# Optimization experiments

Hardware: AMD Instinct MI355X
Metric: run time of the kernel (lower is better)

The kernel has to match this reference:

```python
import jax, jax.numpy as jnp
import numpy as np
import math

B, N, D_IN, D, D_OUT, H = 4, 2048, 128, 128, 256, 4  # D = dim_hidden//2


def _lin(key, din, dout):
    k1, k2 = jax.random.split(key)
    s = 1.0 / math.sqrt(din)
    W = jax.random.uniform(k1, (din, dout), jnp.float32, -s, s)
    b = jax.random.uniform(k2, (dout,), jnp.float32, -s, s)
    return W, b


def setup_inputs() -> dict:
    key = jax.random.key(0)
    ks = jax.random.split(key, 20)
    inp = {"X": jax.random.normal(ks[0], (B, N, D_IN), jnp.float32)}
    # mab dims: (dim_Q, dim_K) -> dim_V=D for each of the 3 MABs
    mab_dims = [(D_IN, D_IN), (D, D), (D, D)]
    ki = 1
    for i, (dq, dk) in enumerate(mab_dims):
        inp[f"m{i}_Wq"], inp[f"m{i}_bq"] = _lin(ks[ki], dq, D); ki += 1
        inp[f"m{i}_Wk"], inp[f"m{i}_bk"] = _lin(ks[ki], dk, D); ki += 1
        inp[f"m{i}_Wv"], inp[f"m{i}_bv"] = _lin(ks[ki], dk, D); ki += 1
        inp[f"m{i}_Wo"], inp[f"m{i}_bo"] = _lin(ks[ki], D, D); ki += 1
    a = math.sqrt(6.0 / (D + 1))  # xavier_uniform for S [1,1,D]
    inp["S"] = jax.random.uniform(ks[ki], (1, 1, D), jnp.float32, -a, a); ki += 1
    inp["pW"], inp["pb"] = _lin(ks[ki], D, D_OUT)
    return inp


def _mab(Q, K, Wq, bq, Wk, bk, Wv, bv, Wo, bo):
    # Linear projections
    Qp = Q @ Wq + bq                       # [B, Nq, D]
    Kp = K @ Wk + bk                       # [B, Nk, D]
    Vp = K @ Wv + bv                       # [B, Nk, D]
    b, nq, dV = Qp.shape
    dh = dV // H
    # torch split(dim_split,2)+cat(0) == head-split on last dim
    Qh = Qp.reshape(b, nq, H, dh)
    Kh = Kp.reshape(b, -1, H, dh)
    Vh = Vp.reshape(b, -1, H, dh)
    # sigmoid attention (no softmax normalizer)
    A = jax.nn.sigmoid(jnp.einsum('bnhd,bmhd->bhnm', Qh, Kh) / jnp.sqrt(jnp.float32(dV)))
    O = Qh + jnp.einsum('bhnm,bmhd->bnhd', A, Vh)
    O = O.reshape(b, nq, dV)
    # residual ReLU-FFN (no LayerNorm since ln=False)
    return O + jax.nn.relu(O @ Wo + bo)


def reference(X,
              m0_Wq, m0_bq, m0_Wk, m0_bk, m0_Wv, m0_bv, m0_Wo, m0_bo,
              m1_Wq, m1_bq, m1_Wk, m1_bk, m1_Wv, m1_bv, m1_Wo, m1_bo,
              m2_Wq, m2_bq, m2_Wk, m2_bk, m2_Wv, m2_bv, m2_Wo, m2_bo,
              S, pW, pb):
    # SAB layer 0: self-attention, dim_in -> D
    Xh = _mab(X, X, m0_Wq, m0_bq, m0_Wk, m0_bk, m0_Wv, m0_bv, m0_Wo, m0_bo)
    # SAB layer 1: D -> D
    Xh = _mab(Xh, Xh, m1_Wq, m1_bq, m1_Wk, m1_bk, m1_Wv, m1_bv, m1_Wo, m1_bo)
    # PMA pooling: seed queries attend over the set
    Sb = jnp.broadcast_to(S, (Xh.shape[0], S.shape[1], S.shape[2]))
    P = _mab(Sb, Xh, m2_Wq, m2_bq, m2_Wk, m2_bk, m2_Wv, m2_bv, m2_Wo, m2_bo)
    # final projection D -> dim_hidden
    return P @ pW + pb  # [B, num_seeds, D_OUT]
```

## Files before the change

### kernel.cpp

```cpp
#include <hip/hip_runtime.h>
#include <hip/hip_bf16.h>

typedef __hip_bfloat16 HB;
typedef __attribute__((ext_vector_type(8))) short short8;
typedef __attribute__((ext_vector_type(4))) short short4v;
typedef __attribute__((ext_vector_type(4))) float f32x4;
typedef __attribute__((ext_vector_type(2))) unsigned int uint2v;
typedef __attribute__((ext_vector_type(4))) unsigned int uint4v;

constexpr int Bn = 4, Nn = 2048, Dm = 128, Hh = 4;
constexpr int MN = Bn * Nn;
constexpr size_t SZ = (size_t)MN * Dm;

static __device__ __forceinline__ short f2bs(float x) {
    __hip_bfloat16 h = __float2bfloat16(x);
    return __builtin_bit_cast(short, h);
}
static __device__ __forceinline__ unsigned short f2bh(float x) {
    return (unsigned short)((__builtin_bit_cast(unsigned int, x) + 0x8000u) >> 16);
}
static __device__ __forceinline__ unsigned int pk2(float lo, float hi) {
    unsigned int a = __builtin_bit_cast(unsigned int, lo) + 0x8000u;
    unsigned int b = __builtin_bit_cast(unsigned int, hi) + 0x8000u;
#if __has_builtin(__builtin_amdgcn_perm)
    return __builtin_amdgcn_perm(b, a, 0x07060302u);
#else
    return (a >> 16) | (b & 0xFFFF0000u);
#endif
}
static __device__ __forceinline__ float ex2(float x) {
#if __has_builtin(__builtin_amdgcn_exp2f)
    return __builtin_amdgcn_exp2f(x);
#else
    return exp2f(x);
#endif
}
#define NSC2 (-0.12751884772864078f)

static __device__ __forceinline__ size_t kh_idx(int row, int col) {
    return ((size_t)((row >> 11) * 4 + (col >> 5)) * 2048 + (row & 2047)) * 32 + (col & 31);
}

__global__ void k_wprep(const float* __restrict__ Wa, const float* __restrict__ Wb,
                        const float* __restrict__ Wc, const float* __restrict__ Wd,
                        const float* __restrict__ We, const float* __restrict__ Wf,
                        const float* __restrict__ Wg, const float* __restrict__ Wh,
                        const float* __restrict__ Wi, const float* __restrict__ Wj,
                        HB* __restrict__ WtAll) {
    const float* src;
    switch (blockIdx.x) {
        case 0: src = Wa; break; case 1: src = Wb; break;
        case 2: src = Wc; break; case 3: src = Wd; break;
        case 4: src = We; break; case 5: src = Wf; break;
        case 6: src = Wg; break; case 7: src = Wh; break;
        case 8: src = Wi; break; default: src = Wj; break;
    }
    HB* dst = WtAll + (size_t)blockIdx.x * 16384;
    #pragma unroll
    for (int it = 0; it < 2; ++it) {
        int idx = blockIdx.y * 512 + it * 256 + threadIdx.x;
        int g = idx >> 7, c = idx & 127;
        short8 p;
        #pragma unroll
        for (int j = 0; j < 8; ++j) p[j] = f2bs(src[(size_t)(g * 8 + j) * 128 + c]);
        *(short8*)((short*)dst + (size_t)idx * 8) = p;
    }
}

template<int NW, int RELU, int NEXTRA, int FUSE>
__global__ __launch_bounds__(512) void k_linm(
        const float* __restrict__ A, const float* __restrict__ extra,
        const HB* __restrict__ Wt0, const float* __restrict__ b0,
        const HB* __restrict__ Wt1, const float* __restrict__ b1,
        const HB* __restrict__ Wt2, const float* __restrict__ b2,
        float* __restrict__ C0, float* __restrict__ C1,
        HB* __restrict__ Qb, HB* __restrict__ Kb, HB* __restrict__ Vt) {
    const int tid = threadIdx.x;
    const int w = tid >> 6, lane = tid & 63, l15 = lane & 15, quad = lane >> 4;
    const int row0 = blockIdx.x * 32 + (w >> 2) * 16;
    const int cbase = (w & 3) * 32;

    short8 af[4];
    #pragma unroll
    for (int kc = 0; kc < 4; ++kc) {
        const float* ap = A + (size_t)(row0 + l15) * 128 + kc * 32 + quad * 8;
        float4 x0 = *(const float4*)ap;
        float4 x1 = *(const float4*)(ap + 4);
        if (NEXTRA) {
            const float* ep = extra + (size_t)(row0 + l15) * 128 + kc * 32 + quad * 8;
            float4 e0 = *(const float4*)ep, e1 = *(const float4*)(ep + 4);
            x0.x += e0.x; x0.y += e0.y; x0.z += e0.z; x0.w += e0.w;
            x1.x += e1.x; x1.y += e1.y; x1.z += e1.z; x1.w += e1.w;
        }
        uint4v u;
        u[0] = pk2(x0.x, x0.y); u[1] = pk2(x0.z, x0.w);
        u[2] = pk2(x1.x, x1.y); u[3] = pk2(x1.z, x1.w);
        af[kc] = __builtin_bit_cast(short8, u);
    }

    f32x4 zero = {0.f, 0.f, 0.f, 0.f};
    #pragma unroll
    for (int ct = 0; ct < 2; ++ct) {
        const int col = cbase + ct * 16 + l15;
        #pragma unroll
        for (int s = 0; s < NW; ++s) {
            const HB* Wt = (s == 0) ? Wt0 : (s == 1) ? Wt1 : Wt2;
            const float* bs = (s == 0) ? b0 : (s == 1) ? b1 : b2;
            f32x4 acc = zero;
            #pragma unroll
            for (int kc = 0; kc < 4; ++kc) {
                short8 bf = *(const short8*)((const short*)Wt + ((size_t)(kc * 4 + quad) * 128 + col) * 8);
                acc = __builtin_amdgcn_mfma_f32_16x16x32_bf16(af[kc], bf, acc, 0, 0, 0);
            }
            float bb = bs[col];
            if (s == 0 || !FUSE) {
                float* Cs = (s == 0) ? C0 : C1;
                #pragma unroll
                for (int r = 0; r < 4; ++r) {
                    int row = row0 + quad * 4 + r;
                    float v = acc[r] + bb;
                    if (RELU && s == 0) {
                        float st = A[(size_t)row * 128 + col];
                        if (NEXTRA) st += extra[(size_t)row * 128 + col];
                        v = fmaxf(v, 0.f) + st;
                    }
                    Cs[(size_t)row * 128 + col] = v;
                    if (FUSE && s == 0)
                        ((unsigned short*)Qb)[(size_t)row * 128 + col] = f2bh(v);
                }
            } else if (s == 1) {
                #pragma unroll
                for (int r = 0; r < 4; ++r) {
                    int row = row0 + quad * 4 + r;
                    ((unsigned short*)Kb)[kh_idx(row, col)] = f2bh(acc[r] + bb);
                }
            } else {
                int b_ = row0 >> 11;
                int mloc = (row0 + quad * 4) & 2047;
                int slotb = (mloc & ~31) + (((mloc & 15) >> 2) << 3) + (((mloc >> 4) & 1) << 2);
                int h_ = col >> 5, dh = col & 31;
                uint2v pv;
                pv[0] = pk2(acc[0] + bb, acc[1] + bb);
                pv[1] = pk2(acc[2] + bb, acc[3] + bb);
                *(short4v*)((short*)Vt + ((size_t)((b_ * 4 + h_) * 32 + dh)) * 2048 + slotb)
                    = __builtin_bit_cast(short4v, pv);
            }
        }
    }
}

template<int NQKV, int FUSE>
__global__ __launch_bounds__(512) void k_fused(
        const float* __restrict__ A, const float* __restrict__ extra,
        const HB* __restrict__ WtO, const float* __restrict__ bO,
        const HB* __restrict__ Wt0, const float* __restrict__ b0,
        const HB* __restrict__ Wt1, const float* __restrict__ b1,
        const HB* __restrict__ Wt2, const float* __restrict__ b2,
        float* __restrict__ C0, float* __restrict__ C1,
        HB* __restrict__ Qb, HB* __restrict__ Kb, HB* __restrict__ Vt) {
    const int tid = threadIdx.x;
    const int w = tid >> 6, lane = tid & 63, l15 = lane & 15, quad = lane >> 4;
    const int lrow0 = (w >> 2) * 16;
    const int row0 = blockIdx.x * 32 + lrow0;
    const int cbase = (w & 3) * 32;

    __shared__ float xs[32 * 132];

    short8 af[4];
    #pragma unroll
    for (int kc = 0; kc < 4; ++kc) {
        const float* ap = A + (size_t)(row0 + l15) * 128 + kc * 32 + quad * 8;
        float4 x0 = *(const float4*)ap;
        float4 x1 = *(const float4*)(ap + 4);
        const float* ep = extra + (size_t)(row0 + l15) * 128 + kc * 32 + quad * 8;
        float4 e0 = *(const float4*)ep, e1 = *(const float4*)(ep + 4);
        x0.x += e0.x; x0.y += e0.y; x0.z += e0.z; x0.w += e0.w;
        x1.x += e1.x; x1.y += e1.y; x1.z += e1.z; x1.w += e1.w;
        uint4v u;
        u[0] = pk2(x0.x, x0.y); u[1] = pk2(x0.z, x0.w);
        u[2] = pk2(x1.x, x1.y); u[3] = pk2(x1.z, x1.w);
        af[kc] = __builtin_bit_cast(short8, u);
    }

    f32x4 zero = {0.f, 0.f, 0.f, 0.f};

    #pragma unroll
    for (int ct = 0; ct < 2; ++ct) {
        const int col = cbase + ct * 16 + l15;
        f32x4 acc = zero;
        #pragma unroll
        for (int kc = 0; kc < 4; ++kc) {
            short8 bf = *(const short8*)((const short*)WtO + ((size_t)(kc * 4 + quad) * 128 + col) * 8);
            acc = __builtin_amdgcn_mfma_f32_16x16x32_bf16(af[kc], bf, acc, 0, 0, 0);
        }
        float bb = bO[col];
        #pragma unroll
        for (int r = 0; r < 4; ++r) {
            int row = row0 + quad * 4 + r;
            float st = A[(size_t)row * 128 + col] + extra[(size_t)row * 128 + col];
            xs[(lrow0 + quad * 4 + r) * 132 + col] = fmaxf(acc[r] + bb, 0.f) + st;
        }
    }
    __syncthreads();

    short8 a2[4];
    {
        const float* xrow = xs + (size_t)(lrow0 + l15) * 132;
        #pragma unroll
        for (int kc = 0; kc < 4; ++kc) {
            f32x4 x0 = *(const f32x4*)(xrow + kc * 32 + quad * 8);
            f32x4 x1 = *(const f32x4*)(xrow + kc * 32 + quad * 8 + 4);
            uint4v u;
            u[0] = pk2(x0[0], x0[1]); u[1] = pk2(x0[2], x0[3]);
            u[2] = pk2(x1[0], x1[1]); u[3] = pk2(x1[2], x1[3]);
            a2[kc] = __builtin_bit_cast(short8, u);
        }
    }

    #pragma unroll
    for (int ct = 0; ct < 2; ++ct) {
        const int col = cbase + ct * 16 + l15;
        #pragma unroll
        for (int s = 0; s < NQKV; ++s) {
            const HB* Wt = (s == 0) ? Wt0 : (s == 1) ? Wt1 : Wt2;
            const float* bs = (s == 0) ? b0 : (s == 1) ? b1 : b2;
            f32x4 acc = zero;
            #pragma unroll
            for (int kc = 0; kc < 4; ++kc) {
                short8 bf = *(const short8*)((const short*)Wt + ((size_t)(kc * 4 + quad) * 128 + col) * 8);
                acc = __builtin_amdgcn_mfma_f32_16x16x32_bf16(a2[kc], bf, acc, 0, 0, 0);
            }
            float bb = bs[col];
            if (s == 0 || !FUSE) {
                float* Cs = (s == 0) ? C0 : C1;
                #pragma unroll
                for (int r = 0; r < 4; ++r) {
                    int row = row0 + quad * 4 + r;
                    float v = acc[r] + bb;
                    Cs[(size_t)row * 128 + col] = v;
                    if (FUSE && s == 0)
                        ((unsigned short*)Qb)[(size_t)row * 128 + col] = f2bh(v);
                }
            } else if (s == 1) {
                #pragma unroll
                for (int r = 0; r < 4; ++r) {
                    int row = row0 + quad * 4 + r;
                    ((unsigned short*)Kb)[kh_idx(row, col)] = f2bh(acc[r] + bb);
                }
            } else {
                int b_ = row0 >> 11;
                int mloc = (row0 + quad * 4) & 2047;
                int slotb = (mloc & ~31) + (((mloc & 15) >> 2) << 3) + (((mloc >> 4) & 1) << 2);
                int h_ = col >> 5, dh = col & 31;
                uint2v pv;
                pv[0] = pk2(acc[0] + bb, acc[1] + bb);
                pv[1] = pk2(acc[2] + bb, acc[3] + bb);
                *(short4v*)((short*)Vt + ((size_t)((b_ * 4 + h_) * 32 + dh)) * 2048 + slotb)
                    = __builtin_bit_cast(short4v, pv);
            }
        }
    }
}

__global__ __launch_bounds__(512, 4) void k_attn4(const HB* __restrict__ Qb, const HB* __restrict__ Kbf,
                                                  const HB* __restrict__ Vt, float* __restrict__ Opart) {
    const int tid = threadIdx.x;
    const int w = tid >> 6, lane = tid & 63, l15 = lane & 15, quad = lane >> 4;
    const int bh = blockIdx.x & 15, qg2 = blockIdx.x >> 4;
    const int b = bh >> 2, h = bh & 3;
    const int q0row = qg2 * 64;

    __shared__ float ldsacc[8][64][36];

    short8 aq[4];
    {
        const short* qp = (const short*)Qb + (size_t)(b * Nn + q0row) * 128 + h * 32 + quad * 8;
        #pragma unroll
        for (int qa = 0; qa < 4; ++qa)
            aq[qa] = *(const short8*)(qp + (size_t)(qa * 16 + l15) * 128);
    }

    f32x4 zero = {0.f, 0.f, 0.f, 0.f};
    f32x4 o[4][2];
    #pragma unroll
    for (int qa = 0; qa < 4; ++qa) { o[qa][0] = zero; o[qa][1] = zero; }

    const short* Kb = (const short*)Kbf + (size_t)bh * Nn * 32;
    const short* Vb = (const short*)Vt + (size_t)bh * 32 * Nn;

    for (int m0 = w * 256; m0 < w * 256 + 256; m0 += 64) {
        short8 kb[4];
        #pragma unroll
        for (int mc = 0; mc < 4; ++mc)
            kb[mc] = *(const short8*)(Kb + (size_t)(m0 + mc * 16 + l15) * 32 + quad * 8);
        short8 vf[2][2];
        #pragma unroll
        for (int t = 0; t < 2; ++t)
            #pragma unroll
            for (int u = 0; u < 2; ++u)
                vf[t][u] = *(const short8*)(Vb + (size_t)(t * 16 + l15) * Nn + m0 + u * 32 + quad * 8);

        #pragma unroll
        for (int qa = 0; qa < 4; ++qa) {
            f32x4 s[4];
            #pragma unroll
            for (int mc = 0; mc < 4; ++mc)
                s[mc] = __builtin_amdgcn_mfma_f32_16x16x32_bf16(kb[mc], aq[qa], zero, 0, 0, 0);
            #pragma unroll
            for (int u = 0; u < 2; ++u) {
                f32x4 lo = s[2 * u], hi = s[2 * u + 1];
                float p0 = __builtin_amdgcn_rcpf(1.f + ex2(lo[0] * NSC2));
                float p1 = __builtin_amdgcn_rcpf(1.f + ex2(lo[1] * NSC2));
                float p2 = __builtin_amdgcn_rcpf(1.f + ex2(lo[2] * NSC2));
                float p3 = __builtin_amdgcn_rcpf(1.f + ex2(lo[3] * NSC2));
                float p4 = __builtin_amdgcn_rcpf(1.f + ex2(hi[0] * NSC2));
                float p5 = __builtin_amdgcn_rcpf(1.f + ex2(hi[1] * NSC2));
                float p6 = __builtin_amdgcn_rcpf(1.f + ex2(hi[2] * NSC2));
                float p7 = __builtin_amdgcn_rcpf(1.f + ex2(hi[3] * NSC2));
                uint4v pu;
                pu[0] = pk2(p0, p1); pu[1] = pk2(p2, p3);
                pu[2] = pk2(p4, p5); pu[3] = pk2(p6, p7);
                short8 pf = __builtin_bit_cast(short8, pu);
                #pragma unroll
                for (int t = 0; t < 2; ++t)
                    o[qa][t] = __builtin_amdgcn_mfma_f32_16x16x32_bf16(vf[t][u], pf, o[qa][t], 0, 0, 0);
            }
        }
    }

    #pragma unroll
    for (int qa = 0; qa < 4; ++qa)
        #pragma unroll
        for (int t = 0; t < 2; ++t)
            *(f32x4*)&ldsacc[w][qa * 16 + l15][t * 16 + quad * 4] = o[qa][t];
    __syncthreads();
    const int row = tid >> 3, cc = (tid & 7) * 4;
    f32x4 sum = zero;
    #pragma unroll
    for (int ww = 0; ww < 8; ++ww) {
        f32x4 r = *(f32x4*)&ldsacc[ww][row][cc];
        sum += r;
    }
    *(f32x4*)(Opart + (size_t)(b * Nn + q0row + row) * 128 + h * 32 + cc) = sum;
}

__global__ void k_pma2(const float* __restrict__ S, const float* __restrict__ Wq, const float* __restrict__ bq,
                       const float* __restrict__ Kp, const float* __restrict__ Vp,
                       float* __restrict__ P0part) {
    const int bh = blockIdx.x, b = bh >> 2, h = bh & 3;
    const int ms = blockIdx.y;
    const int tid = threadIdx.x;
    __shared__ float4 qs4[8];
    float* qs = (float*)qs4;
    if (tid < 32) {
        float a = bq[h * 32 + tid];
        for (int k = 0; k < 128; ++k)
            a = fmaf(S[k], Wq[k * Dm + h * 32 + tid], a);
        qs[tid] = a;
    }
    __syncthreads();

    float4 q[8];
    #pragma unroll
    for (int i = 0; i < 8; ++i) q[i] = qs4[i];

    const size_t base = (size_t)b * Nn * Dm + h * 32;
    const int m = ms * 256 + tid;

    const float4* kp = (const float4*)(Kp + base + (size_t)m * Dm);
    const float4* vp = (const float4*)(Vp + base + (size_t)m * Dm);
    float d0 = 0.f, d1 = 0.f, d2 = 0.f, d3 = 0.f;
    #pragma unroll
    for (int c = 0; c < 8; c += 4) {
        float4 k0 = kp[c+0], k1 = kp[c+1], k2 = kp[c+2], k3 = kp[c+3];
        d0 += q[c+0].x*k0.x + q[c+0].y*k0.y + q[c+0].z*k0.z + q[c+0].w*k0.w;
        d1 += q[c+1].x*k1.x + q[c+1].y*k1.y + q[c+1].z*k1.z + q[c+1].w*k1.w;
        d2 += q[c+2].x*k2.x + q[c+2].y*k2.y + q[c+2].z*k2.z + q[c+2].w*k2.w;
        d3 += q[c+3].x*k3.x + q[c+3].y*k3.y + q[c+3].z*k3.z + q[c+3].w*k3.w;
    }
    float dot = (d0 + d1) + (d2 + d3);
    float a = __builtin_amdgcn_rcpf(1.f + ex2(dot * NSC2));
    float4 acc[8];
    #pragma unroll
    for (int c = 0; c < 8; ++c) {
        float4 vv = vp[c];
        acc[c].x = a * vv.x; acc[c].y = a * vv.y; acc[c].z = a * vv.z; acc[c].w = a * vv.w;
    }
    #pragma unroll
    for (int off = 1; off < 64; off <<= 1) {
        #pragma unroll
        for (int c = 0; c < 8; ++c) {
            acc[c].x += __shfl_xor(acc[c].x, off);
            acc[c].y += __shfl_xor(acc[c].y, off);
            acc[c].z += __shfl_xor(acc[c].z, off);
            acc[c].w += __shfl_xor(acc[c].w, off);
        }
    }
    __shared__ float red[4][32];
    const int wave = tid >> 6, lane = tid & 63;
    if (lane == 0) {
        #pragma unroll
        for (int c = 0; c < 8; ++c) {
            red[wave][c*4+0] = acc[c].x; red[wave][c*4+1] = acc[c].y;
            red[wave][c*4+2] = acc[c].z; red[wave][c*4+3] = acc[c].w;
        }
    }
    __syncthreads();
    if (tid < 32) {
        float t = (red[0][tid] + red[1][tid]) + (red[2][tid] + red[3][tid]);
        if (ms == 0) t += qs[tid];
        P0part[ms * 512 + b * 128 + h * 32 + tid] = t;
    }
}

__global__ __launch_bounds__(256) void k_tail(const float* __restrict__ P0part,
                                              const float* __restrict__ W23, const float* __restrict__ b23,
                                              const float* __restrict__ pW, const float* __restrict__ pb,
                                              float* __restrict__ out) {
    const int b = blockIdx.x, tid = threadIdx.x;
    __shared__ float staged[128], pp[128];
    if (tid < 128) {
        float s = 0.f;
        #pragma unroll
        for (int ms = 0; ms < 8; ++ms) s += P0part[ms * 512 + b * 128 + tid];
        staged[tid] = s;
    }
    __syncthreads();
    if (tid < 128) {
        float acc = b23[tid];
        #pragma unroll 8
        for (int k = 0; k < 128; ++k)
            acc = fmaf(staged[k], W23[k * 128 + tid], acc);
        pp[tid] = fmaxf(acc, 0.f) + staged[tid];
    }
    __syncthreads();
    float a = pb[tid];
    #pragma unroll 8
    for (int k = 0; k < 128; ++k)
        a = fmaf(pp[k], pW[k * 256 + tid], a);
    out[b * 256 + tid] = a;
}

extern "C" void kernel_launch(void* const* d_in, const int* in_sizes, int n_in,
                              void* d_out, int out_size, void* d_ws, size_t ws_size,
                              hipStream_t stream) {
    const float* X = (const float*)d_in[0];
    auto W = [&](int i) { return (const float*)d_in[i]; };
    float* ws = (float*)d_ws;

    float* s0 = ws + 0 * SZ;
    float* s1 = ws + 1 * SZ;
    float* s2 = ws + 2 * SZ;
    float* s3 = ws + 3 * SZ;
    HB*    B4  = (HB*)(ws + 4 * SZ);
    HB*    Qb  = B4;
    HB*    Kbf = B4 + SZ;
    HB*    Vt  = B4 + 2 * SZ;
    HB*    WtAll = B4 + 3 * SZ;
    auto Wt = [&](int idx) { return (const HB*)(WtAll + (size_t)idx * 16384); };
    float* P0part = s1;

    const int GLM = MN / 32;
    const int attn_blocks = 512;
    dim3 wprep_grid(10, 4);
    dim3 pma_grid(Bn * Hh, 8);
    const float* nul = nullptr;

    k_wprep<<<wprep_grid, 256, 0, stream>>>(W(1), W(3), W(5), W(7), W(9), W(11), W(13), W(15),
                                            W(19), W(21), WtAll);

    k_linm<3,0,0,1><<<GLM, 512, 0, stream>>>(X, nul, Wt(0), W(2), Wt(1), W(4), Wt(2), W(6),
                                             s0, nullptr, Qb, Kbf, Vt);
    k_attn4<<<attn_blocks, 512, 0, stream>>>(Qb, Kbf, Vt, s2);

    k_fused<3,1><<<GLM, 512, 0, stream>>>(s0, s2, Wt(3), W(8),
                                          Wt(4), W(10), Wt(5), W(12), Wt(6), W(14),
                                          s1, nullptr, Qb, Kbf, Vt);
    k_attn4<<<attn_blocks, 512, 0, stream>>>(Qb, Kbf, Vt, s2);

    k_fused<2,0><<<GLM, 512, 0, stream>>>(s1, s2, Wt(7), W(16),
                                          Wt(8), W(20), Wt(9), W(22), nullptr, nul,
                                          s0, s3, nullptr, nullptr, nullptr);

    k_pma2<<<pma_grid, 256, 0, stream>>>((const float*)d_in[25], W(17), W(18), s0, s3, P0part);
    k_tail<<<Bn, 256, 0, stream>>>(P0part, W(23), W(24), (const float*)d_in[26], (const float*)d_in[27],
                                   (float*)d_out);
}
```

Before: 208.5 us.

## Split fused FFN+QKV kernels into smaller linear kernels with bf16 intermediate

Replaces the fused Wo-FFN plus next-layer projection kernels with two launches of a generic linear kernel. The new kernel uses 16-row blocks with a column-split grid and 256 threads, which raises the block count for more parallelism. The FFN output is stored as bf16 and read directly as the MFMA A operand. This adds two kernel launches and a global round trip for the intermediate in exchange for more blocks and less per-block work. The PMA kernel now uses blockIdx.y directly in place of the ms variable.

```diff
diff --git a/kernel.cpp b/kernel.cpp
--- a/kernel.cpp
+++ b/kernel.cpp
@@ -67,197 +67,106 @@
     }
 }
 
-template<int NW, int RELU, int NEXTRA, int FUSE>
-__global__ __launch_bounds__(512) void k_linm(
-        const float* __restrict__ A, const float* __restrict__ extra,
+template<int NW, int NEXTRA, int FUSE, int ABF, int OUTB>
+__global__ __launch_bounds__(256) void k_lin2(
+        const void* __restrict__ Av, const float* __restrict__ extra,
         const HB* __restrict__ Wt0, const float* __restrict__ b0,
         const HB* __restrict__ Wt1, const float* __restrict__ b1,
         const HB* __restrict__ Wt2, const float* __restrict__ b2,
         float* __restrict__ C0, float* __restrict__ C1,
-        HB* __restrict__ Qb, HB* __restrict__ Kb, HB* __restrict__ Vt) {
+        HB* __restrict__ Xb, HB* __restrict__ Qb, HB* __restrict__ Kb, HB* __restrict__ Vt) {
     const int tid = threadIdx.x;
     const int w = tid >> 6, lane = tid & 63, l15 = lane & 15, quad = lane >> 4;
-    const int row0 = blockIdx.x * 32 + (w >> 2) * 16;
-    const int cbase = (w & 3) * 32;
+    const int row0 = blockIdx.x * 16;
+    const int col = blockIdx.y * 64 + w * 16 + l15;
+    const float* Af = (const float*)Av;
 
     short8 af[4];
-    #pragma unroll
-    for (int kc = 0; kc < 4; ++kc) {
-        const float* ap = A + (size_t)(row0 + l15) * 128 + kc * 32 + quad * 8;
-        float4 x0 = *(const float4*)ap;
-        float4 x1 = *(const float4*)(ap + 4);
-        if (NEXTRA) {
-            const float* ep = extra + (size_t)(row0 + l15) * 128 + kc * 32 + quad * 8;
-            float4 e0 = *(const float4*)ep, e1 = *(const float4*)(ep + 4);
-            x0.x += e0.x; x0.y += e0.y; x0.z += e0.z; x0.w += e0.w;
-            x1.x += e1.x; x1.y += e1.y; x1.z += e1.z; x1.w += e1.w;
-        }
-        uint4v u;
-        u[0] = pk2(x0.x, x0.y); u[1] = pk2(x0.z, x0.w);
-        u[2] = pk2(x1.x, x1.y); u[3] = pk2(x1.z, x1.w);
-        af[kc] = __builtin_bit_cast(short8, u);
+    if (ABF) {
+        const short* ab = (const short*)Av + (size_t)(row0 + l15) * 128 + quad * 8;
+        #pragma unroll
+        for (int kc = 0; kc < 4; ++kc)
+            af[kc] = *(const short8*)(ab + kc * 32);
+    } else {
+        #pragma unroll
+        for (int kc = 0; kc < 4; ++kc) {
+            const float* ap = Af + (size_t)(row0 + l15) * 128 + kc * 32 + quad * 8;
+            float4 x0 = *(const float4*)ap;
+            float4 x1 = *(const float4*)(ap + 4);
+            if (NEXTRA) {
+                const float* ep = extra + (size_t)(row0 + l15) * 128 + kc * 32 + quad * 8;
+                float4 e0 = *(const float4*)ep, e1 = *(const float4*)(ep + 4);
+                x0.x += e0.x; x0.y += e0.y; x0.z += e0.z; x0.w += e0.w;
+                x1.x += e1.x; x1.y += e1.y; x1.z += e1.z; x1.w += e1.w;
+            }
+            uint4v u;
+            u[0] = pk2(x0.x, x0.y); u[1] = pk2(x0.z, x0.w);
+            u[2] = pk2(x1.x, x1.y); u[3] = pk2(x1.z, x1.w);
+            af[kc] = __builtin_bit_cast(short8, u);
+        }
     }
 
     f32x4 zero = {0.f, 0.f, 0.f, 0.f};
     #pragma unroll
-    for (int ct = 0; ct < 2; ++ct) {
-        const int col = cbase + ct * 16 + l15;
-        #pragma unroll
-        for (int s = 0; s < NW; ++s) {
-            const HB* Wt = (s == 0) ? Wt0 : (s == 1) ? Wt1 : Wt2;
-            const float* bs = (s == 0) ? b0 : (s == 1) ? b1 : b2;
-            f32x4 acc = zero;
-            #pragma unroll
-            for (int kc = 0; kc < 4; ++kc) {
-                short8 bf = *(const short8*)((const short*)Wt + ((size_t)(kc * 4 + quad) * 128 + col) * 8);
-                acc = __builtin_amdgcn_mfma_f32_16x16x32_bf16(af[kc], bf, acc, 0, 0, 0);
-            }
-            float bb = bs[col];
-            if (s == 0 || !FUSE) {
-                float* Cs = (s == 0) ? C0 : C1;
+    for (int s = 0; s < NW; ++s) {
+        const HB* Wt = (s == 0) ? Wt0 : (s == 1) ? Wt1 : Wt2;
+        const float* bs = (s == 0) ? b0 : (s == 1) ? b1 : b2;
+        f32x4 acc = zero;
+        #pragma unroll
+        for (int kc = 0; kc < 4; ++kc) {
+            short8 bf = *(const short8*)((const short*)Wt + ((size_t)(kc * 4 + quad) * 128 + col) * 8);
+            acc = __builtin_amdgcn_mfma_f32_16x16x32_bf16(af[kc], bf, acc, 0, 0, 0);
+        }
+        float bb = bs[col];
+        if (s == 0) {
+            if (OUTB) {
+                #pragma unroll
+                for (int r = 0; r < 4; ++r) {
+                    int row = row0 + quad * 4 + r;
+                    float st = Af[(size_t)row * 128 + col];
+                    if (NEXTRA) st += extra[(size_t)row * 128 + col];
+                    float v = fmaxf(acc[r] + bb, 0.f) + st;
+                    ((unsigned short*)Xb)[(size_t)row * 128 + col] = f2bh(v);
+                }
+            } else if (FUSE) {
                 #pragma unroll
                 for (int r = 0; r < 4; ++r) {
                     int row = row0 + quad * 4 + r;
                     float v = acc[r] + bb;
-                    if (RELU && s == 0) {
-                        float st = A[(size_t)row * 128 + col];
-                        if (NEXTRA) st += extra[(size_t)row * 128 + col];
-                        v = fmaxf(v, 0.f) + st;
-                    }
-                    Cs[(size_t)row * 128 + col] = v;
-                    if (FUSE && s == 0)
-                        ((unsigned short*)Qb)[(size_t)row * 128 + col] = f2bh(v);
+                    C0[(size_t)row * 128 + col] = v;
+                    ((unsigned short*)Qb)[(size_t)row * 128 + col] = f2bh(v);
                 }
-            } else if (s == 1) {
+            } else {
+                #pragma unroll
+                for (int r = 0; r < 4; ++r) {
+                    int row = row0 + quad * 4 + r;
+                    C0[(size_t)row * 128 + col] = acc[r] + bb;
+                }
+            }
+        } else if (s == 1) {
+            if (FUSE) {
                 #pragma unroll
                 for (int r = 0; r < 4; ++r) {
                     int row = row0 + quad * 4 + r;
                     ((unsigned short*)Kb)[kh_idx(row, col)] = f2bh(acc[r] + bb);
                 }
             } else {
-                int b_ = row0 >> 11;
-                int mloc = (row0 + quad * 4) & 2047;
-                int slotb = (mloc & ~31) + (((mloc & 15) >> 2) << 3) + (((mloc >> 4) & 1) << 2);
-                int h_ = col >> 5, dh = col & 31;
-                uint2v pv;
-                pv[0] = pk2(acc[0] + bb, acc[1] + bb);
-                pv[1] = pk2(acc[2] + bb, acc[3] + bb);
-                *(short4v*)((short*)Vt + ((size_t)((b_ * 4 + h_) * 32 + dh)) * 2048 + slotb)
-                    = __builtin_bit_cast(short4v, pv);
-            }
-        }
-    }
-}
-
-template<int NQKV, int FUSE>
-__global__ __launch_bounds__(512) void k_fused(
-        const float* __restrict__ A, const float* __restrict__ extra,
-        const HB* __restrict__ WtO, const float* __restrict__ bO,
-        const HB* __restrict__ Wt0, const float* __restrict__ b0,
-        const HB* __restrict__ Wt1, const float* __restrict__ b1,
-        const HB* __restrict__ Wt2, const float* __restrict__ b2,
-        float* __restrict__ C0, float* __restrict__ C1,
-        HB* __restrict__ Qb, HB* __restrict__ Kb, HB* __restrict__ Vt) {
-    const int tid = threadIdx.x;
-    const int w = tid >> 6, lane = tid & 63, l15 = lane & 15, quad = lane >> 4;
-    const int lrow0 = (w >> 2) * 16;
-    const int row0 = blockIdx.x * 32 + lrow0;
-    const int cbase = (w & 3) * 32;
-
-    __shared__ float xs[32 * 132];
-
-    short8 af[4];
-    #pragma unroll
-    for (int kc = 0; kc < 4; ++kc) {
-        const float* ap = A + (size_t)(row0 + l15) * 128 + kc * 32 + quad * 8;
-        float4 x0 = *(const float4*)ap;
-        float4 x1 = *(const float4*)(ap + 4);
-        const float* ep = extra + (size_t)(row0 + l15) * 128 + kc * 32 + quad * 8;
-        float4 e0 = *(const float4*)ep, e1 = *(const float4*)(ep + 4);
-        x0.x += e0.x; x0.y += e0.y; x0.z += e0.z; x0.w += e0.w;
-        x1.x += e1.x; x1.y += e1.y; x1.z += e1.z; x1.w += e1.w;
-        uint4v u;
-        u[0] = pk2(x0.x, x0.y); u[1] = pk2(x0.z, x0.w);
-        u[2] = pk2(x1.x, x1.y); u[3] = pk2(x1.z, x1.w);
-        af[kc] = __builtin_bit_cast(short8, u);
-    }
-
-    f32x4 zero = {0.f, 0.f, 0.f, 0.f};
-
-    #pragma unroll
-    for (int ct = 0; ct < 2; ++ct) {
-        const int col = cbase + ct * 16 + l15;
-        f32x4 acc = zero;
-        #pragma unroll
-        for (int kc = 0; kc < 4; ++kc) {
-            short8 bf = *(const short8*)((const short*)WtO + ((size_t)(kc * 4 + quad) * 128 + col) * 8);
-            acc = __builtin_amdgcn_mfma_f32_16x16x32_bf16(af[kc], bf, acc, 0, 0, 0);
-        }
-        float bb = bO[col];
-        #pragma unroll
-        for (int r = 0; r < 4; ++r) {
-            int row = row0 + quad * 4 + r;
-            float st = A[(size_t)row * 128 + col] + extra[(size_t)row * 128 + col];
-            xs[(lrow0 + quad * 4 + r) * 132 + col] = fmaxf(acc[r] + bb, 0.f) + st;
-        }
-    }
-    __syncthreads();
-
-    short8 a2[4];
-    {
-        const float* xrow = xs + (size_t)(lrow0 + l15) * 132;
-        #pragma unroll
-        for (int kc = 0; kc < 4; ++kc) {
-            f32x4 x0 = *(const f32x4*)(xrow + kc * 32 + quad * 8);
-            f32x4 x1 = *(const f32x4*)(xrow + kc * 32 + quad * 8 + 4);
-            uint4v u;
-            u[0] = pk2(x0[0], x0[1]); u[1] = pk2(x0[2], x0[3]);
-            u[2] = pk2(x1[0], x1[1]); u[3] = pk2(x1[2], x1[3]);
-            a2[kc] = __builtin_bit_cast(short8, u);
-        }
-    }
-
-    #pragma unroll
-    for (int ct = 0; ct < 2; ++ct) {
-        const int col = cbase + ct * 16 + l15;
-        #pragma unroll
-        for (int s = 0; s < NQKV; ++s) {
-            const HB* Wt = (s == 0) ? Wt0 : (s == 1) ? Wt1 : Wt2;
-            const float* bs = (s == 0) ? b0 : (s == 1) ? b1 : b2;
-            f32x4 acc = zero;
-            #pragma unroll
-            for (int kc = 0; kc < 4; ++kc) {
-                short8 bf = *(const short8*)((const short*)Wt + ((size_t)(kc * 4 + quad) * 128 + col) * 8);
-                acc = __builtin_amdgcn_mfma_f32_16x16x32_bf16(a2[kc], bf, acc, 0, 0, 0);
-            }
-            float bb = bs[col];
-            if (s == 0 || !FUSE) {
-                float* Cs = (s == 0) ? C0 : C1;
                 #pragma unroll
                 for (int r = 0; r < 4; ++r) {
                     int row = row0 + quad * 4 + r;
-                    float v = acc[r] + bb;
-                    Cs[(size_t)row * 128 + col] = v;
-                    if (FUSE && s == 0)
-                        ((unsigned short*)Qb)[(size_t)row * 128 + col] = f2bh(v);
+                    C1[(size_t)row * 128 + col] = acc[r] + bb;
                 }
-            } else if (s == 1) {
-                #pragma unroll
-                for (int r = 0; r < 4; ++r) {
-                    int row = row0 + quad * 4 + r;
-                    ((unsigned short*)Kb)[kh_idx(row, col)] = f2bh(acc[r] + bb);
-                }
-            } else {
-                int b_ = row0 >> 11;
-                int mloc = (row0 + quad * 4) & 2047;
-                int slotb = (mloc & ~31) + (((mloc & 15) >> 2) << 3) + (((mloc >> 4) & 1) << 2);
-                int h_ = col >> 5, dh = col & 31;
-                uint2v pv;
-                pv[0] = pk2(acc[0] + bb, acc[1] + bb);
-                pv[1] = pk2(acc[2] + bb, acc[3] + bb);
-                *(short4v*)((short*)Vt + ((size_t)((b_ * 4 + h_) * 32 + dh)) * 2048 + slotb)
-                    = __builtin_bit_cast(short4v, pv);
             }
+        } else {
+            int b_ = row0 >> 11;
+            int mloc = (row0 + quad * 4) & 2047;
+            int slotb = (mloc & ~31) + (((mloc & 15) >> 2) << 3) + (((mloc >> 4) & 1) << 2);
+            int h_ = col >> 5, dh = col & 31;
+            uint2v pv;
+            pv[0] = pk2(acc[0] + bb, acc[1] + bb);
+            pv[1] = pk2(acc[2] + bb, acc[3] + bb);
+            *(short4v*)((short*)Vt + ((size_t)((b_ * 4 + h_) * 32 + dh)) * 2048 + slotb)
+                = __builtin_bit_cast(short4v, pv);
         }
     }
 }
@@ -365,7 +274,7 @@
     for (int i = 0; i < 8; ++i) q[i] = qs4[i];
 
     const size_t base = (size_t)b * Nn * Dm + h * 32;
-    const int m = ms * 256 + tid;
+    const int m = blockIdx.y * 256 + tid;
 
     const float4* kp = (const float4*)(Kp + base + (size_t)m * Dm);
     const float4* vp = (const float4*)(Vp + base + (size_t)m * Dm);
@@ -408,8 +317,8 @@
     __syncthreads();
     if (tid < 32) {
         float t = (red[0][tid] + red[1][tid]) + (red[2][tid] + red[3][tid]);
-        if (ms == 0) t += qs[tid];
-        P0part[ms * 512 + b * 128 + h * 32 + tid] = t;
+        if (blockIdx.y == 0) t += qs[tid];
+        P0part[blockIdx.y * 512 + b * 128 + h * 32 + tid] = t;
     }
 }
 
@@ -456,31 +365,35 @@
     HB*    Qb  = B4;
     HB*    Kbf = B4 + SZ;
     HB*    Vt  = B4 + 2 * SZ;
-    HB*    WtAll = B4 + 3 * SZ;
+    HB*    Xb  = B4 + 3 * SZ;
+    HB*    WtAll = B4 + 4 * SZ;
     auto Wt = [&](int idx) { return (const HB*)(WtAll + (size_t)idx * 16384); };
     float* P0part = s1;
 
-    const int GLM = MN / 32;
+    dim3 lin_grid(MN / 16, 2);
     const int attn_blocks = 512;
     dim3 wprep_grid(10, 4);
     dim3 pma_grid(Bn * Hh, 8);
     const float* nul = nullptr;
+    HB* nulh = nullptr;
 
     k_wprep<<<wprep_grid, 256, 0, stream>>>(W(1), W(3), W(5), W(7), W(9), W(11), W(13), W(15),
                                             W(19), W(21), WtAll);
 
-    k_linm<3,0,0,1><<<GLM, 512, 0, stream>>>(X, nul, Wt(0), W(2), Wt(1), W(4), Wt(2), W(6),
-                                             s0, nullptr, Qb, Kbf, Vt);
+    k_lin2<3,0,1,0,0><<<lin_grid, 256, 0, stream>>>(X, nul, Wt(0), W(2), Wt(1), W(4), Wt(2), W(6),
+                                                    s0, nullptr, nulh, Qb, Kbf, Vt);
     k_attn4<<<attn_blocks, 512, 0, stream>>>(Qb, Kbf, Vt, s2);
-
-    k_fused<3,1><<<GLM, 512, 0, stream>>>(s0, s2, Wt(3), W(8),
-                                          Wt(4), W(10), Wt(5), W(12), Wt(6), W(14),
-                                          s1, nullptr, Qb, Kbf, Vt);
+    k_lin2<1,1,0,0,1><<<lin_grid, 256, 0, stream>>>(s0, s2, Wt(3), W(8), nullptr, nul, nullptr, nul,
+                                                    nullptr, nullptr, Xb, nulh, nulh, nulh);
+
+    k_lin2<3,0,1,1,0><<<lin_grid, 256, 0, stream>>>(Xb, nul, Wt(4), W(10), Wt(5), W(12), Wt(6), W(14),
+                                                    s1, nullptr, nulh, Qb, Kbf, Vt);
     k_attn4<<<attn_blocks, 512, 0, stream>>>(Qb, Kbf, Vt, s2);
-
-    k_fused<2,0><<<GLM, 512, 0, stream>>>(s1, s2, Wt(7), W(16),
-                                          Wt(8), W(20), Wt(9), W(22), nullptr, nul,
-                                          s0, s3, nullptr, nullptr, nullptr);
+    k_lin2<1,1,0,0,1><<<lin_grid, 256, 0, stream>>>(s1, s2, Wt(7), W(16), nullptr, nul, nullptr, nul,
+                                                    nullptr, nullptr, Xb, nulh, nulh, nulh);
+
+    k_lin2<2,0,0,1,0><<<lin_grid, 256, 0, stream>>>(Xb, nul, Wt(8), W(20), Wt(9), W(22), nullptr, nul,
+                                                    s0, s3, nulh, nulh, nulh, nulh);
 
     k_pma2<<<pma_grid, 256, 0, stream>>>((const float*)d_in[25], W(17), W(18), s0, s3, P0part);
     k_tail<<<Bn, 256, 0, stream>>>(P0part, W(23), W(24), (const float*)d_in[26], (const float*)d_in[27],
```

Result: slower. 220.7 us (+5.8%).
